# Performance work log

Measured on AMD Instinct MI355X. Metric: run time of the kernel, lower is better.

## Reference

```python
import jax, jax.numpy as jnp
import numpy as np

EPS = 1e-4  # matches normalize()/pixel_norm eps in the torch source
MP_T = 0.3  # mp_add mixing coefficient


def _weight_norm_1x1(w):
    # w: [out, in, 1, 1]; normalize each output filter (dims 1..3), alpha = 1/sqrt(fan_in),
    # then divide by sqrt(fan_in) as in Conv2d.forward (eval mode: no in-place copy).
    fan_in = w.shape[1] * w.shape[2] * w.shape[3]
    inv_sqrt_fan = np.float32(1.0 / np.sqrt(fan_in))
    n = jnp.sqrt(jnp.sum(w * w, axis=(1, 2, 3), keepdims=True))
    w_hat = w / (EPS + inv_sqrt_fan * n)
    return w_hat * inv_sqrt_fan


def _conv1x1(x, w):
    # 1x1 conv == channel GEMM
    return jnp.einsum('oc,bchw->bohw', _weight_norm_1x1(w)[:, :, 0, 0], x)


def _pixel_norm_last(x):
    # x / sqrt(mean(x^2, axis=-1) + eps)
    ms = jnp.mean(x * x, axis=-1, keepdims=True)
    return x * jax.lax.rsqrt(ms + EPS)


def setup_inputs() -> dict:
    key = jax.random.key(0)
    k1, k2, k3 = jax.random.split(key, 3)
    x = jax.random.normal(k1, (2, 256, 64, 64), dtype=jnp.float32)
    w_qkv = jax.random.normal(k2, (768, 256, 1, 1), dtype=jnp.float32)
    w_out = jax.random.normal(k3, (256, 256, 1, 1), dtype=jnp.float32)
    return {"x": x, "w_qkv": w_qkv, "w_out": w_out, "num_heads": 8}


def reference(x, w_qkv, w_out, num_heads):
    b, c, h, w = x.shape
    head_dim = c // num_heads
    qkv = _conv1x1(x, w_qkv)                      # [b, 3c, h, w]
    q, k, v = jnp.split(qkv, 3, axis=1)           # each [b, c, h, w]

    def to_heads(t):
        # [b, c, h, w] -> [b, heads, hw, head_dim]
        return t.reshape(b, num_heads, head_dim, h * w).transpose(0, 1, 3, 2)

    q = _pixel_norm_last(to_heads(q))
    k = _pixel_norm_last(to_heads(k))
    v = _pixel_norm_last(to_heads(v))

    scale = np.float32(1.0 / np.sqrt(head_dim))
    scores = jnp.einsum('bhqd,bhkd->bhqk', q, k) * scale
    attn = jax.nn.softmax(scores, axis=-1)
    y = jnp.einsum('bhqk,bhkd->bhqd', attn, v)    # [b, heads, hw, head_dim]
    y = y.transpose(0, 1, 3, 2).reshape(b, c, h, w)
    y = _conv1x1(y, w_out)

    # mp_add(x, y, t=0.3)
    t = np.float32(MP_T)
    inv_scale = np.float32(1.0 / np.sqrt(MP_T ** 2 + (1.0 - MP_T) ** 2))
    return ((1.0 - t) * x + t * y) * inv_scale
```

## Files before the change

### kernel.cpp

```cpp
#include <hip/hip_runtime.h>
#include <hip/hip_bf16.h>
#include <math.h>

#define S 4096
#define CIN 256
#define C3 768
#define NH 8
#define HD 32
#define KSPLIT 4

static constexpr float EPS = 1e-4f;

typedef __attribute__((ext_vector_type(8))) __bf16 bf16x8;
typedef __attribute__((ext_vector_type(4))) float f32x4;
typedef __attribute__((ext_vector_type(16))) float f32x16;
typedef __attribute__((ext_vector_type(4))) unsigned u32x4;

static inline __device__ ushort f2bf(float f) {
  unsigned u = __float_as_uint(f);
  return (ushort)((u + 0x7fffu + ((u >> 16) & 1u)) >> 16);
}
static inline __device__ float bf2f(ushort u) {
  return __uint_as_float((unsigned)u << 16);
}

static inline __device__ unsigned cvt_pk_bf16(float lo, float hi) {
  unsigned r;
  asm("v_cvt_pk_bf16_f32 %0, %1, %2" : "=v"(r) : "v"(lo), "v"(hi));
  return r;
}
static inline __device__ void plane32_swap(unsigned& a, unsigned& b) {
  asm("v_permlane32_swap_b32 %0, %1" : "+v"(a), "+v"(b));
}

#define EXP2 __builtin_amdgcn_exp2f

static inline __device__ void s_to_pf(const f32x16 s, bf16x8& plo, bf16x8& phi,
                                      float& lacc) {
  float e0 = EXP2(s[0]), e1 = EXP2(s[1]), e2 = EXP2(s[2]), e3 = EXP2(s[3]);
  float e4 = EXP2(s[4]), e5 = EXP2(s[5]), e6 = EXP2(s[6]), e7 = EXP2(s[7]);
  float e8 = EXP2(s[8]), e9 = EXP2(s[9]), e10 = EXP2(s[10]), e11 = EXP2(s[11]);
  float e12 = EXP2(s[12]), e13 = EXP2(s[13]), e14 = EXP2(s[14]), e15 = EXP2(s[15]);
  lacc += (((e0 + e1) + (e2 + e3)) + ((e4 + e5) + (e6 + e7))) +
          (((e8 + e9) + (e10 + e11)) + ((e12 + e13) + (e14 + e15)));
  unsigned c0 = cvt_pk_bf16(e0, e1);
  unsigned c1 = cvt_pk_bf16(e2, e3);
  unsigned c2 = cvt_pk_bf16(e4, e5);
  unsigned c3 = cvt_pk_bf16(e6, e7);
  plane32_swap(c0, c2);
  plane32_swap(c1, c3);
  u32x4 lo4 = {c0, c1, c2, c3};
  plo = __builtin_bit_cast(bf16x8, lo4);
  unsigned c4 = cvt_pk_bf16(e8, e9);
  unsigned c5 = cvt_pk_bf16(e10, e11);
  unsigned c6 = cvt_pk_bf16(e12, e13);
  unsigned c7 = cvt_pk_bf16(e14, e15);
  plane32_swap(c4, c6);
  plane32_swap(c5, c7);
  u32x4 hi4 = {c4, c5, c6, c7};
  phi = __builtin_bit_cast(bf16x8, hi4);
}

__global__ __launch_bounds__(256) void wnorm_kernel(const float* __restrict__ w_qkv,
                                                    const float* __restrict__ w_out,
                                                    ushort* __restrict__ wqb,
                                                    ushort* __restrict__ wob) {
  const int row = blockIdx.x * 4 + (threadIdx.x >> 6);
  const int lane = threadIdx.x & 63;
  const bool is_q = row < C3;
  const float* wr = (is_q ? w_qkv + (size_t)row * CIN : w_out + (size_t)(row - C3) * CIN);
  float v0 = wr[lane], v1 = wr[lane + 64], v2 = wr[lane + 128], v3 = wr[lane + 192];
  float ss = v0 * v0 + v1 * v1 + v2 * v2 + v3 * v3;
  #pragma unroll
  for (int off = 32; off > 0; off >>= 1) ss += __shfl_down(ss, off, 64);
  ss = __shfl(ss, 0, 64);
  const float scale = 1.0f / (sqrtf(ss) + 16.0f * EPS);
  ushort* whr = (is_q ? wqb + (size_t)row * CIN : wob + (size_t)(row - C3) * CIN);
  whr[lane] = f2bf(v0 * scale);
  whr[lane + 64] = f2bf(v1 * scale);
  whr[lane + 128] = f2bf(v2 * scale);
  whr[lane + 192] = f2bf(v3 * scale);
}

__global__ __launch_bounds__(256) void xt_kernel(const float* __restrict__ X,
                                                 ushort* __restrict__ Xt) {
  const int b = blockIdx.z;
  const int s0 = blockIdx.x * 64, c0 = blockIdx.y * 64;
  __shared__ ushort T[64][72];
  const int tc = threadIdx.x >> 4;
  const int ts = threadIdx.x & 15;
  #pragma unroll
  for (int i = 0; i < 4; i++) {
    const float4 v = *(const float4*)&X[((size_t)(b * CIN + c0 + tc + 16 * i)) * S + s0 + ts * 4];
    ushort4 u;
    u.x = f2bf(v.x); u.y = f2bf(v.y); u.z = f2bf(v.z); u.w = f2bf(v.w);
    *(ushort4*)&T[tc + 16 * i][ts * 4] = u;
  }
  __syncthreads();
  #pragma unroll
  for (int i = 0; i < 4; i++) {
    const int sr = tc + 16 * i;
    ushort4 u;
    u.x = T[ts * 4 + 0][sr];
    u.y = T[ts * 4 + 1][sr];
    u.z = T[ts * 4 + 2][sr];
    u.w = T[ts * 4 + 3][sr];
    *(ushort4*)&Xt[((size_t)b * S + s0 + sr) * CIN + c0 + ts * 4] = u;
  }
}

__global__ __launch_bounds__(256) void conv1_fused_kernel(const ushort* __restrict__ W,
                                                          const ushort* __restrict__ Bm,
                                                          ushort* __restrict__ Qn,
                                                          ushort* __restrict__ Kn,
                                                          ushort* __restrict__ Vt) {
  const int b = blockIdx.z;
  const int wid = threadIdx.x >> 6, lane = threadIdx.x & 63;
  const int col = lane & 15, quad = lane >> 4;
  const int m0 = blockIdx.y * 64 + (wid >> 1) * 32;
  const int n0 = blockIdx.x * 128 + (wid & 1) * 64;
  const ushort* Bb = Bm + (size_t)b * S * CIN;
  f32x4 acc[2][4] = {};
  #pragma unroll
  for (int k0 = 0; k0 < CIN; k0 += 32) {
    bf16x8 af[2], bf[4];
    #pragma unroll
    for (int mi = 0; mi < 2; mi++)
      af[mi] = *(const bf16x8*)&W[(size_t)(m0 + mi * 16 + col) * CIN + k0 + quad * 8];
    #pragma unroll
    for (int ni = 0; ni < 4; ni++)
      bf[ni] = *(const bf16x8*)&Bb[(size_t)(n0 + ni * 16 + col) * CIN + k0 + quad * 8];
    #pragma unroll
    for (int mi = 0; mi < 2; mi++)
      #pragma unroll
      for (int ni = 0; ni < 4; ni++)
        acc[mi][ni] = __builtin_amdgcn_mfma_f32_16x16x32_bf16(af[mi], bf[ni], acc[mi][ni], 0, 0, 0);
  }

  const int g = m0 >> 5;
  const int h = g & 7;
  float rn[4];
  #pragma unroll
  for (int ni = 0; ni < 4; ni++) {
    float ss = 0.f;
    #pragma unroll
    for (int mi = 0; mi < 2; mi++)
      #pragma unroll
      for (int r = 0; r < 4; r++) ss += acc[mi][ni][r] * acc[mi][ni][r];
    ss += __shfl_xor(ss, 16, 64);
    ss += __shfl_xor(ss, 32, 64);
    rn[ni] = rsqrtf(ss * (1.0f / HD) + EPS);
    if (g < 8) rn[ni] *= 0.2550348190698169f;
  }

  if (g < 8) {
    ushort* dst = Qn + (size_t)(b * NH + h) * S * HD;
    #pragma unroll
    for (int mi = 0; mi < 2; mi++)
      #pragma unroll
      for (int ni = 0; ni < 4; ni++) {
        ushort4 u;
        u.x = f2bf(acc[mi][ni][0] * rn[ni]);
        u.y = f2bf(acc[mi][ni][1] * rn[ni]);
        u.z = f2bf(acc[mi][ni][2] * rn[ni]);
        u.w = f2bf(acc[mi][ni][3] * rn[ni]);
        *(ushort4*)&dst[(size_t)(n0 + ni * 16 + col) * HD + mi * 16 + quad * 4] = u;
      }
  } else if (g < 16) {
    ushort* dst = Kn + (size_t)(b * NH + h) * S * HD + (size_t)(n0 >> 5) * 1024;
    #pragma unroll
    for (int mi = 0; mi < 2; mi++)
      #pragma unroll
      for (int ni = 0; ni < 4; ni++) {
        ushort4 u;
        u.x = f2bf(acc[mi][ni][0] * rn[ni]);
        u.y = f2bf(acc[mi][ni][1] * rn[ni]);
        u.z = f2bf(acc[mi][ni][2] * rn[ni]);
        u.w = f2bf(acc[mi][ni][3] * rn[ni]);
        *(ushort4*)&dst[(ni >> 1) * 1024 + mi * 512 + ((ni & 1) * 16 + col) * 16 +
                        (quad >> 1) * 8 + (quad & 1) * 4] = u;
      }
  } else {
    ushort* dst = Vt + (size_t)(b * NH + h) * HD * S + (size_t)(n0 >> 6) * 2048;
    #pragma unroll
    for (int mi = 0; mi < 2; mi++)
      #pragma unroll
      for (int ni = 0; ni < 4; ni++)
        #pragma unroll
        for (int r = 0; r < 4; r++)
          dst[ni * 512 + (mi * 16 + quad * 4 + r) * 16 + col] =
              f2bf(acc[mi][ni][r] * rn[ni]);
  }
}

__global__ __launch_bounds__(256, 4) void attn_kernel(const ushort* __restrict__ Qn,
                                                      const ushort* __restrict__ Kn,
                                                      const ushort* __restrict__ Vt,
                                                      ushort* __restrict__ accPb,
                                                      float* __restrict__ lP) {
  const int NWG = (S / 256) * NH * KSPLIT * 2;
  const int bid = blockIdx.x;
  const int id = (bid & 7) * (NWG / 8) + (bid >> 3);
  const int qt = id & 15;
  const int grp = id >> 4;
  const int h = grp & 7;
  const int kp = (grp >> 3) & (KSPLIT - 1);
  const int b = (grp >> 3) / KSPLIT;
  const int wid = threadIdx.x >> 6, lane = threadIdx.x & 63;
  const int ln = lane & 31, hi = lane >> 5;
  const int qA = qt * 256 + wid * 64;
  const int qB = qA + 32;

  const ushort* Qh = Qn + (size_t)(b * NH + h) * S * HD;

  bf16x8 qfA0 = *(const bf16x8*)&Qh[(size_t)(qA + ln) * HD + hi * 8];
  bf16x8 qfA1 = *(const bf16x8*)&Qh[(size_t)(qA + ln) * HD + 16 + hi * 8];
  bf16x8 qfB0 = *(const bf16x8*)&Qh[(size_t)(qB + ln) * HD + hi * 8];
  bf16x8 qfB1 = *(const bf16x8*)&Qh[(size_t)(qB + ln) * HD + 16 + hi * 8];

  const f32x16 z = {};
  f32x16 accA = {}, accB = {};
  float laccA = 0.f, laccB = 0.f;

  const int kt0 = kp * (S / KSPLIT);
  const int loff = (ln * 2 + hi) * 8;
  const ushort* Kp = Kn + (size_t)(b * NH + h) * S * HD + (size_t)kt0 * 32 + loff;
  const ushort* Vp = Vt + (size_t)(b * NH + h) * HD * S + (size_t)kt0 * 32 + loff;

  bf16x8 kf0 = *(const bf16x8*)&Kp[0];
  bf16x8 kf1 = *(const bf16x8*)&Kp[512];
  bf16x8 vf0 = *(const bf16x8*)&Vp[0];
  bf16x8 vf1 = *(const bf16x8*)&Vp[512];

  #pragma unroll 1
  for (int it = 0; it < S / KSPLIT / 32; ++it) {
    f32x16 sA = __builtin_amdgcn_mfma_f32_32x32x16_bf16(kf0, qfA0, z, 0, 0, 0);
    sA = __builtin_amdgcn_mfma_f32_32x32x16_bf16(kf1, qfA1, sA, 0, 0, 0);
    f32x16 sB = __builtin_amdgcn_mfma_f32_32x32x16_bf16(kf0, qfB0, z, 0, 0, 0);
    sB = __builtin_amdgcn_mfma_f32_32x32x16_bf16(kf1, qfB1, sB, 0, 0, 0);
    Kp += 1024;
    kf0 = *(const bf16x8*)&Kp[0];
    kf1 = *(const bf16x8*)&Kp[512];

    bf16x8 pfA0, pfA1;
    s_to_pf(sA, pfA0, pfA1, laccA);
    accA = __builtin_amdgcn_mfma_f32_32x32x16_bf16(vf0, pfA0, accA, 0, 0, 0);
    accA = __builtin_amdgcn_mfma_f32_32x32x16_bf16(vf1, pfA1, accA, 0, 0, 0);

    bf16x8 pfB0, pfB1;
    s_to_pf(sB, pfB0, pfB1, laccB);
    accB = __builtin_amdgcn_mfma_f32_32x32x16_bf16(vf0, pfB0, accB, 0, 0, 0);
    accB = __builtin_amdgcn_mfma_f32_32x32x16_bf16(vf1, pfB1, accB, 0, 0, 0);

    Vp += 1024;
    vf0 = *(const bf16x8*)&Vp[0];
    vf1 = *(const bf16x8*)&Vp[512];
  }

  ushort* ap = accPb + ((size_t)((kp * 2 + b) * NH + h)) * S * HD;
  const size_t rowA = (size_t)(qA + ln) * HD;
  const size_t rowB = (size_t)(qB + ln) * HD;
  #pragma unroll
  for (int g = 0; g < 4; g++) {
    uint2 u;
    u.x = cvt_pk_bf16(accA[4 * g + 0], accA[4 * g + 1]);
    u.y = cvt_pk_bf16(accA[4 * g + 2], accA[4 * g + 3]);
    *(uint2*)&ap[rowA + g * 8 + hi * 4] = u;
    uint2 v;
    v.x = cvt_pk_bf16(accB[4 * g + 0], accB[4 * g + 1]);
    v.y = cvt_pk_bf16(accB[4 * g + 2], accB[4 * g + 3]);
    *(uint2*)&ap[rowB + g * 8 + hi * 4] = v;
  }
  const float lsA = laccA + __shfl_xor(laccA, 32, 64);
  const float lsB = laccB + __shfl_xor(laccB, 32, 64);
  if (hi == 0) {
    float* lp = lP + ((size_t)((kp * 2 + b) * NH + h)) * S;
    lp[qA + ln] = lsA;
    lp[qB + ln] = lsB;
  }
}

__global__ __launch_bounds__(256) void combine_kernel(const ushort* __restrict__ accPb,
                                                      const float* __restrict__ lP,
                                                      ushort* __restrict__ Yt) {
  const int tid = blockIdx.x * 256 + threadIdx.x;
  const int dg = tid & 7;
  const int q = (tid >> 3) & (S - 1);
  const int h = (tid >> 15) & 7;
  const int b = tid >> 18;
  const size_t i0 = ((size_t)(b * NH + h)) * S + q;
  const size_t part = (size_t)2 * NH * S;
  float sx = 0.f, sy = 0.f, sz = 0.f, sw = 0.f, L = 0.f;
  #pragma unroll
  for (int p = 0; p < KSPLIT; p++) {
    const ushort4 a = *(const ushort4*)&accPb[(size_t)p * part * HD + i0 * HD + dg * 4];
    sx += bf2f(a.x); sy += bf2f(a.y); sz += bf2f(a.z); sw += bf2f(a.w);
    L += lP[(size_t)p * part + i0];
  }
  const float rl = 1.0f / L;
  ushort4 o;
  o.x = f2bf(sx * rl);
  o.y = f2bf(sy * rl);
  o.z = f2bf(sz * rl);
  o.w = f2bf(sw * rl);
  *(ushort4*)&Yt[((size_t)b * S + q) * CIN + h * HD + dg * 4] = o;
}

__global__ __launch_bounds__(256) void conv2_kernel(const ushort* __restrict__ W,
                                                    const ushort* __restrict__ Bm,
                                                    const float* __restrict__ RES,
                                                    float* __restrict__ OUT) {
  const int b = blockIdx.z;
  const int wid = threadIdx.x >> 6, lane = threadIdx.x & 63;
  const int col = lane & 15, quad = lane >> 4;
  const int m0 = blockIdx.y * 64 + (wid >> 1) * 32;
  const int n0 = blockIdx.x * 64 + (wid & 1) * 32;
  const ushort* Bb = Bm + (size_t)b * S * CIN;
  f32x4 acc[2][2] = {};
  #pragma unroll
  for (int k0 = 0; k0 < CIN; k0 += 32) {
    bf16x8 af[2], bf[2];
    #pragma unroll
    for (int mi = 0; mi < 2; mi++)
      af[mi] = *(const bf16x8*)&W[(size_t)(m0 + mi * 16 + col) * CIN + k0 + quad * 8];
    #pragma unroll
    for (int ni = 0; ni < 2; ni++)
      bf[ni] = *(const bf16x8*)&Bb[(size_t)(n0 + ni * 16 + col) * CIN + k0 + quad * 8];
    #pragma unroll
    for (int mi = 0; mi < 2; mi++)
      #pragma unroll
      for (int ni = 0; ni < 2; ni++)
        acc[mi][ni] = __builtin_amdgcn_mfma_f32_16x16x32_bf16(af[mi], bf[ni], acc[mi][ni], 0, 0, 0);
  }
  const float tc = 0.3f, om = 0.7f, inv = 1.3130643285972254f;
  #pragma unroll
  for (int mi = 0; mi < 2; mi++)
    #pragma unroll
    for (int ni = 0; ni < 2; ni++)
      #pragma unroll
      for (int r = 0; r < 4; r++) {
        const size_t idx = ((size_t)(b * CIN + m0 + mi * 16 + quad * 4 + r)) * S + n0 + ni * 16 + col;
        OUT[idx] = (om * RES[idx] + tc * acc[mi][ni][r]) * inv;
      }
}

extern "C" void kernel_launch(void* const* d_in, const int* in_sizes, int n_in,
                              void* d_out, int out_size, void* d_ws, size_t ws_size,
                              hipStream_t stream) {
  const float* x = (const float*)d_in[0];
  const float* w_qkv = (const float*)d_in[1];
  const float* w_out = (const float*)d_in[2];
  float* out = (float*)d_out;

  ushort* p = (ushort*)d_ws;
  ushort* wqb = p; p += (size_t)C3 * CIN;
  ushort* wob = p; p += (size_t)CIN * CIN;
  ushort* Qn = p; p += (size_t)2 * NH * S * HD;
  ushort* Kn = p; p += (size_t)2 * NH * S * HD;
  ushort* Vt = p; p += (size_t)2 * NH * S * HD;
  ushort* Yt = p; p += (size_t)2 * S * CIN;
  ushort* R = p; p += (size_t)KSPLIT * 2 * NH * S * HD;
  ushort* Xt = R;
  ushort* accPb = R;
  float* lP = (float*)p;

  wnorm_kernel<<<(C3 + CIN) / 4, 256, 0, stream>>>(w_qkv, w_out, wqb, wob);
  xt_kernel<<<dim3(S / 64, CIN / 64, 2), 256, 0, stream>>>(x, Xt);
  conv1_fused_kernel<<<dim3(S / 128, C3 / 64, 2), 256, 0, stream>>>(wqb, Xt, Qn, Kn, Vt);
  attn_kernel<<<(S / 256) * NH * KSPLIT * 2, 256, 0, stream>>>(Qn, Kn, Vt, accPb, lP);
  combine_kernel<<<2048, 256, 0, stream>>>(accPb, lP, Yt);
  conv2_kernel<<<dim3(S / 64, CIN / 64, 2), 256, 0, stream>>>(wob, Yt, x, out);
}
```

Before: 152.8 us.

## Store GEMM operands in 16x32 tile-blocked layout for contiguous MFMA fragment loads

The normalized weights, the transposed bf16 input and the attention output Yt are now written in a blocked layout. Each 16-row by 32-column tile is stored as one contiguous 512-element chunk. Both conv GEMM kernels index this layout, so each wavefront's fragment load reads one contiguous 1KB block instead of 16 rows strided by CIN. The aim is better coalescing and fewer cache lines touched per MFMA operand load, which requires that every producer and consumer agree on the new layout.

```diff
diff --git a/kernel.cpp b/kernel.cpp
--- a/kernel.cpp
+++ b/kernel.cpp
@@ -34,6 +34,7 @@
 }
 
 #define EXP2 __builtin_amdgcn_exp2f
+
 
 static inline __device__ void s_to_pf(const f32x16 s, bf16x8& plo, bf16x8& phi,
                                       float& lacc) {
@@ -68,18 +69,23 @@
   const int row = blockIdx.x * 4 + (threadIdx.x >> 6);
   const int lane = threadIdx.x & 63;
   const bool is_q = row < C3;
-  const float* wr = (is_q ? w_qkv + (size_t)row * CIN : w_out + (size_t)(row - C3) * CIN);
-  float v0 = wr[lane], v1 = wr[lane + 64], v2 = wr[lane + 128], v3 = wr[lane + 192];
-  float ss = v0 * v0 + v1 * v1 + v2 * v2 + v3 * v3;
+  const int r2 = is_q ? row : row - C3;
+  const float* wr = (is_q ? w_qkv : w_out) + (size_t)r2 * CIN;
+  float v[4];
+  #pragma unroll
+  for (int i = 0; i < 4; i++) v[i] = wr[lane + 64 * i];
+  float ss = v[0] * v[0] + v[1] * v[1] + v[2] * v[2] + v[3] * v[3];
   #pragma unroll
   for (int off = 32; off > 0; off >>= 1) ss += __shfl_down(ss, off, 64);
   ss = __shfl(ss, 0, 64);
   const float scale = 1.0f / (sqrtf(ss) + 16.0f * EPS);
-  ushort* whr = (is_q ? wqb + (size_t)row * CIN : wob + (size_t)(row - C3) * CIN);
-  whr[lane] = f2bf(v0 * scale);
-  whr[lane + 64] = f2bf(v1 * scale);
-  whr[lane + 128] = f2bf(v2 * scale);
-  whr[lane + 192] = f2bf(v3 * scale);
+  ushort* whr = (is_q ? wqb : wob);
+  #pragma unroll
+  for (int i = 0; i < 4; i++) {
+    const int c = lane + 64 * i;
+    whr[((size_t)(r2 >> 4) * (CIN / 32) + (c >> 5)) * 512 + (r2 & 15) * 32 + (c & 31)] =
+        f2bf(v[i] * scale);
+  }
 }
 
 __global__ __launch_bounds__(256) void xt_kernel(const float* __restrict__ X,
@@ -100,12 +106,15 @@
   #pragma unroll
   for (int i = 0; i < 4; i++) {
     const int sr = tc + 16 * i;
+    const int s = s0 + sr;
+    const int c = c0 + ts * 4;
     ushort4 u;
     u.x = T[ts * 4 + 0][sr];
     u.y = T[ts * 4 + 1][sr];
     u.z = T[ts * 4 + 2][sr];
     u.w = T[ts * 4 + 3][sr];
-    *(ushort4*)&Xt[((size_t)b * S + s0 + sr) * CIN + c0 + ts * 4] = u;
+    *(ushort4*)&Xt[(((size_t)b * (S / 16) + (s >> 4)) * (CIN / 32) + (c >> 5)) * 512 +
+                   (s & 15) * 32 + (c & 31)] = u;
   }
 }
 
@@ -119,17 +128,18 @@
   const int col = lane & 15, quad = lane >> 4;
   const int m0 = blockIdx.y * 64 + (wid >> 1) * 32;
   const int n0 = blockIdx.x * 128 + (wid & 1) * 64;
-  const ushort* Bb = Bm + (size_t)b * S * CIN;
+  const ushort* Bb = Bm + (size_t)b * (S / 16) * (CIN / 32) * 512;
+  const int lofs = col * 32 + quad * 8;
   f32x4 acc[2][4] = {};
   #pragma unroll
   for (int k0 = 0; k0 < CIN; k0 += 32) {
     bf16x8 af[2], bf[4];
     #pragma unroll
     for (int mi = 0; mi < 2; mi++)
-      af[mi] = *(const bf16x8*)&W[(size_t)(m0 + mi * 16 + col) * CIN + k0 + quad * 8];
+      af[mi] = *(const bf16x8*)&W[((size_t)(m0 / 16 + mi) * (CIN / 32) + (k0 >> 5)) * 512 + lofs];
     #pragma unroll
     for (int ni = 0; ni < 4; ni++)
-      bf[ni] = *(const bf16x8*)&Bb[(size_t)(n0 + ni * 16 + col) * CIN + k0 + quad * 8];
+      bf[ni] = *(const bf16x8*)&Bb[((size_t)(n0 / 16 + ni) * (CIN / 32) + (k0 >> 5)) * 512 + lofs];
     #pragma unroll
     for (int mi = 0; mi < 2; mi++)
       #pragma unroll
@@ -303,7 +313,8 @@
   o.y = f2bf(sy * rl);
   o.z = f2bf(sz * rl);
   o.w = f2bf(sw * rl);
-  *(ushort4*)&Yt[((size_t)b * S + q) * CIN + h * HD + dg * 4] = o;
+  *(ushort4*)&Yt[(((size_t)b * (S / 16) + (q >> 4)) * (CIN / 32) + h) * 512 +
+                 (q & 15) * 32 + dg * 4] = o;
 }
 
 __global__ __launch_bounds__(256) void conv2_kernel(const ushort* __restrict__ W,
@@ -315,17 +326,18 @@
   const int col = lane & 15, quad = lane >> 4;
   const int m0 = blockIdx.y * 64 + (wid >> 1) * 32;
   const int n0 = blockIdx.x * 64 + (wid & 1) * 32;
-  const ushort* Bb = Bm + (size_t)b * S * CIN;
+  const ushort* Bb = Bm + (size_t)b * (S / 16) * (CIN / 32) * 512;
+  const int lofs = col * 32 + quad * 8;
   f32x4 acc[2][2] = {};
   #pragma unroll
   for (int k0 = 0; k0 < CIN; k0 += 32) {
     bf16x8 af[2], bf[2];
     #pragma unroll
     for (int mi = 0; mi < 2; mi++)
-      af[mi] = *(const bf16x8*)&W[(size_t)(m0 + mi * 16 + col) * CIN + k0 + quad * 8];
+      af[mi] = *(const bf16x8*)&W[((size_t)(m0 / 16 + mi) * (CIN / 32) + (k0 >> 5)) * 512 + lofs];
     #pragma unroll
     for (int ni = 0; ni < 2; ni++)
-      bf[ni] = *(const bf16x8*)&Bb[(size_t)(n0 + ni * 16 + col) * CIN + k0 + quad * 8];
+      bf[ni] = *(const bf16x8*)&Bb[((size_t)(n0 / 16 + ni) * (CIN / 32) + (k0 >> 5)) * 512 + lofs];
     #pragma unroll
     for (int mi = 0; mi < 2; mi++)
       #pragma unroll
```

New measurement: 144.6 us. -5.4%, faster.
